# Kernel optimization log

Measured on AMD Instinct MI355X. Metric: run time of the kernel, lower is better.

Reference implementation:

```python
import jax, jax.numpy as jnp
import numpy as np

B, T, D, H = 4, 2048, 1024, 16
HD = D // H  # 64
EPS = 1e-5

def _layernorm(x, g, b):
    mu = jnp.mean(x, axis=-1, keepdims=True)
    var = jnp.var(x, axis=-1, keepdims=True)
    return (x - mu) * jax.lax.rsqrt(var + EPS) * g + b

def setup_inputs() -> dict:
    key = jax.random.key(0)
    ks = jax.random.split(key, 8)
    s = D ** -0.5
    return {
        "x":  jax.random.normal(ks[0], (B, T, D), jnp.float32),
        "Wq": jax.random.normal(ks[1], (H, D, HD), jnp.float32) * s,
        "Wk": jax.random.normal(ks[2], (H, D, HD), jnp.float32) * s,
        "Wv": jax.random.normal(ks[3], (H, D, HD), jnp.float32) * s,
        "Wp": jax.random.normal(ks[4], (D, D), jnp.float32) * s,
        "bp": jnp.zeros((D,), jnp.float32),
        "W1": jax.random.normal(ks[5], (D, 4 * D), jnp.float32) * s,
        "b1": jnp.zeros((4 * D,), jnp.float32),
        "W2": jax.random.normal(ks[6], (4 * D, D), jnp.float32) * (4 * D) ** -0.5,
        "b2": jnp.zeros((D,), jnp.float32),
        "g1": jnp.ones((D,), jnp.float32),
        "be1": jnp.zeros((D,), jnp.float32),
        "g2": jnp.ones((D,), jnp.float32),
        "be2": jnp.zeros((D,), jnp.float32),
    }

def reference(x, Wq, Wk, Wv, Wp, bp, W1, b1, W2, b2, g1, be1, g2, be2):
    # --- pre-LN causal MHA (all heads batched; torch code loops per head) ---
    h = _layernorm(x, g1, be1)                       # [B,T,D]
    q = jnp.einsum('btd,hdk->bhtk', h, Wq)
    k = jnp.einsum('btd,hdk->bhtk', h, Wk)
    v = jnp.einsum('btd,hdk->bhtk', h, Wv)
    scores = jnp.einsum('bhtk,bhsk->bhts', q, k) * (HD ** -0.5)
    causal = jnp.tril(jnp.ones((T, T), bool))
    scores = jnp.where(causal, scores, -jnp.inf)
    w = jax.nn.softmax(scores, axis=-1)              # [B,H,T,T]
    o = jnp.einsum('bhts,bhsk->bhtk', w, v)          # [B,H,T,HD]
    o = o.transpose(0, 2, 1, 3).reshape(x.shape[0], x.shape[1], D)  # concat heads
    x = x + o @ Wp + bp                              # residual 1
    # --- pre-LN FFN ---
    h2 = _layernorm(x, g2, be2)
    ff = jax.nn.relu(h2 @ W1 + b1) @ W2 + b2
    return x + ff
```

## Files before the change

kernel.cpp:

```cpp
#include <hip/hip_runtime.h>
#include <hip/hip_bf16.h>
#include <math.h>

#define Bsz 4
#define Tsz 2048
#define Dsz 1024
#define Hn  16
#define HDs 64

typedef __attribute__((ext_vector_type(8))) short bf16x8;
typedef __attribute__((ext_vector_type(4))) float f32x4;

typedef const __attribute__((address_space(1))) void gvoid;
typedef __attribute__((address_space(3))) void lvoid;

__device__ __forceinline__ void async_copy16(const short* g, short* l) {
    __builtin_amdgcn_global_load_lds((gvoid*)g, (lvoid*)l, 16, 0, 0);
}

__device__ __forceinline__ short f2bf(float x) {
    __hip_bfloat16 h = __float2bfloat16(x);
    return *reinterpret_cast<short*>(&h);
}

__device__ __forceinline__ unsigned int pack_bf16(float hi, float lo) {
    unsigned int uh = __float_as_uint(hi) + 0x8000u;
    unsigned int ul = __float_as_uint(lo) + 0x8000u;
    return __builtin_amdgcn_perm(uh, ul, 0x07060302u);
}

__device__ __forceinline__ size_t headed_idx(int m, int c) {
    int b = m >> 11, t = m & 2047, h = c >> 6, kc = c & 63;
    return (((size_t)(b * Hn + h) * Tsz + t) << 6) + kc;
}

__global__ __launch_bounds__(256) void ln_kernel(const float* __restrict__ x,
                                                 const float* __restrict__ g,
                                                 const float* __restrict__ beta,
                                                 short* __restrict__ out)
{
    const int row = blockIdx.x;
    const float* xr = x + (size_t)row * Dsz;
    float v[4];
    float s = 0.f, s2 = 0.f;
#pragma unroll
    for (int i = 0; i < 4; ++i) {
        v[i] = xr[threadIdx.x + 256 * i];
        s += v[i];
        s2 += v[i] * v[i];
    }
#pragma unroll
    for (int off = 32; off; off >>= 1) {
        s  += __shfl_xor(s,  off);
        s2 += __shfl_xor(s2, off);
    }
    __shared__ float red[8];
    const int wave = threadIdx.x >> 6;
    if ((threadIdx.x & 63) == 0) { red[wave * 2] = s; red[wave * 2 + 1] = s2; }
    __syncthreads();
    s  = red[0] + red[2] + red[4] + red[6];
    s2 = red[1] + red[3] + red[5] + red[7];
    const float mu  = s * (1.f / Dsz);
    const float var = s2 * (1.f / Dsz) - mu * mu;
    const float rs  = rsqrtf(var + 1e-5f);
    short* orow = out + (size_t)row * Dsz;
#pragma unroll
    for (int i = 0; i < 4; ++i) {
        int col = threadIdx.x + 256 * i;
        orow[col] = f2bf((v[i] - mu) * rs * g[col] + beta[col]);
    }
}

__global__ __launch_bounds__(256) void transpose_cvt(
    const float* __restrict__ in, short* __restrict__ outp, int R, int C)
{
    __shared__ float tile[32][33];
    const int r0 = blockIdx.y * 32, c0 = blockIdx.x * 32;
    const size_t so = (size_t)blockIdx.z * R * C;
    const int tx = threadIdx.x & 31, ty = threadIdx.x >> 5;
    const float* ip = in + so;
    short* op = outp + so;
#pragma unroll
    for (int i = 0; i < 4; ++i)
        tile[ty + i * 8][tx] = ip[(size_t)(r0 + ty + i * 8) * C + c0 + tx];
    __syncthreads();
#pragma unroll
    for (int i = 0; i < 4; ++i)
        op[(size_t)(c0 + ty + i * 8) * R + r0 + tx] = f2bf(tile[tx][ty + i * 8]);
}

__global__ __launch_bounds__(256) void transpose_cvt_qkv(
    const float* __restrict__ Wq, const float* __restrict__ Wk,
    const float* __restrict__ Wv, short* __restrict__ outp)
{
    __shared__ float tile[32][33];
    const int z = blockIdx.z;
    const float* in = (z < 16) ? Wq : (z < 32) ? Wk : Wv;
    const int zz = z & 15;
    const int r0 = blockIdx.y * 32, c0 = blockIdx.x * 32;
    const int tx = threadIdx.x & 31, ty = threadIdx.x >> 5;
    const float* ip = in + (size_t)zz * (1024 * 64);
    short* op = outp + (size_t)z * (1024 * 64);
#pragma unroll
    for (int i = 0; i < 4; ++i)
        tile[ty + i * 8][tx] = ip[(size_t)(r0 + ty + i * 8) * 64 + c0 + tx];
    __syncthreads();
#pragma unroll
    for (int i = 0; i < 4; ++i)
        op[(size_t)(c0 + ty + i * 8) * 1024 + r0 + tx] = f2bf(tile[tx][ty + i * 8]);
}

template <int EPI>
__global__ __launch_bounds__(256) void gemm_mfma(
    const short* __restrict__ A, const short* __restrict__ Bt,
    const float* __restrict__ bias, const float* __restrict__ resid,
    float* __restrict__ Cf, short* __restrict__ Cb0,
    short* __restrict__ Cb1, short* __restrict__ Cb2,
    int M, int N, int K, float scale)
{
    __shared__ short As[2][128 * 32];
    __shared__ short Bs[2][128 * 32];
    const int tid  = threadIdx.x;
    const int lane = tid & 63, wave = tid >> 6;
    const int quad = lane >> 4, l16 = lane & 15;

    const int lin = blockIdx.y * gridDim.x + blockIdx.x;
    const int xcd = lin & 7;
    const int s   = lin >> 3;
    const int my  = xcd * 8 + (s & 7);
    const int nx  = s >> 3;
    const int m0 = my * 128, n0 = nx * 128;

    const int wm = (wave >> 1) * 64, wn = (wave & 1) * 64;

    f32x4 acc[4][4];
#pragma unroll
    for (int i = 0; i < 4; ++i)
#pragma unroll
        for (int j = 0; j < 4; ++j) acc[i][j] = f32x4{0.f, 0.f, 0.f, 0.f};

    const short* gA = A  + (size_t)(m0 + wave * 32 + (lane >> 2)) * K + (lane & 3) * 8;
    const short* gB = Bt + (size_t)(n0 + wave * 32 + (lane >> 2)) * K + (lane & 3) * 8;
    const size_t rstep = (size_t)16 * K;
    const int woff = wave * 1024;

    async_copy16(gA,         &As[0][woff]);
    async_copy16(gA + rstep, &As[0][woff + 512]);
    async_copy16(gB,         &Bs[0][woff]);
    async_copy16(gB + rstep, &Bs[0][woff + 512]);
    gA += 32; gB += 32;
    __syncthreads();

    int cur = 0;
    for (int k0 = 0; k0 < K; k0 += 32) {
        if (k0 + 32 < K) {
            const int nxt = cur ^ 1;
            async_copy16(gA,         &As[nxt][woff]);
            async_copy16(gA + rstep, &As[nxt][woff + 512]);
            async_copy16(gB,         &Bs[nxt][woff]);
            async_copy16(gB + rstep, &Bs[nxt][woff + 512]);
            gA += 32; gB += 32;
        }
        bf16x8 af[4], bfr[4];
#pragma unroll
        for (int mt = 0; mt < 4; ++mt)
            af[mt] = *(const bf16x8*)(&As[cur][(wm + mt * 16 + l16) * 32 + quad * 8]);
#pragma unroll
        for (int nt = 0; nt < 4; ++nt)
            bfr[nt] = *(const bf16x8*)(&Bs[cur][(wn + nt * 16 + l16) * 32 + quad * 8]);
#pragma unroll
        for (int mt = 0; mt < 4; ++mt)
#pragma unroll
            for (int nt = 0; nt < 4; ++nt)
                acc[mt][nt] = __builtin_amdgcn_mfma_f32_16x16x32_bf16(
                    af[mt], bfr[nt], acc[mt][nt], 0, 0, 0);
        __syncthreads();
        cur ^= 1;
    }

#pragma unroll
    for (int mt = 0; mt < 4; ++mt) {
#pragma unroll
        for (int nt = 0; nt < 4; ++nt) {
#pragma unroll
            for (int r = 0; r < 4; ++r) {
                const int m = m0 + wm + mt * 16 + quad * 4 + r;
                const int c = n0 + wn + nt * 16 + l16;
                float val = acc[mt][nt][r];
                if (EPI == 0) {
                    const int sel = c >> 10, cl = c & 1023;
                    if (sel == 0)
                        Cb0[headed_idx(m, cl)] = f2bf(val * scale);
                    else if (sel == 1)
                        Cb1[headed_idx(m, cl)] = f2bf(val);
                    else {
                        int b = m >> 11, t = m & 2047;
                        size_t idx = ((((size_t)((b << 4) | (cl >> 6)) << 6) | (cl & 63)) << 11) | t;
                        Cb2[idx] = f2bf(val);
                    }
                } else if (EPI == 2) {
                    size_t idx = (size_t)m * N + c;
                    Cf[idx] = val + bias[c] + resid[idx];
                } else {
                    float v2 = val + bias[c];
                    Cb0[(size_t)m * N + c] = f2bf(v2 > 0.f ? v2 : 0.f);
                }
            }
        }
    }
}

__global__ __launch_bounds__(256) void gemm_n64(
    const short* __restrict__ A, const short* __restrict__ Bt,
    const float* __restrict__ bias, const float* __restrict__ resid,
    float* __restrict__ Cf, int M, int N, int K)
{
    __shared__ short As[2][128 * 64];
    __shared__ short Bs[2][64 * 64];
    const int tid  = threadIdx.x;
    const int lane = tid & 63, wave = tid >> 6;
    const int quad = lane >> 4, l16 = lane & 15;

    const int lin = blockIdx.y * 16 + blockIdx.x;
    const int xcd = lin & 7;
    const int s   = lin >> 3;
    const int m0  = (xcd * 8 + (s & 7)) * 128;
    const int n0  = (s >> 3) * 64;

    const int wm = (wave >> 1) * 64, wn = (wave & 1) * 32;

    f32x4 acc[4][2];
#pragma unroll
    for (int i = 0; i < 4; ++i)
#pragma unroll
        for (int j = 0; j < 2; ++j) acc[i][j] = f32x4{0.f, 0.f, 0.f, 0.f};

    const short* gA[4];
    const short* gB[2];
    int dA[4], dB[2];
#pragma unroll
    for (int i = 0; i < 4; ++i) {
        const int sl = tid + 256 * i, r = sl >> 3, g = (sl & 7) ^ (r & 7);
        gA[i] = A + (size_t)(m0 + r) * K + g * 8;
        dA[i] = sl * 8;
    }
#pragma unroll
    for (int i = 0; i < 2; ++i) {
        const int sl = tid + 256 * i, r = sl >> 3, g = (sl & 7) ^ (r & 7);
        gB[i] = Bt + (size_t)(n0 + r) * K + g * 8;
        dB[i] = sl * 8;
    }

#pragma unroll
    for (int i = 0; i < 4; ++i) { async_copy16(gA[i], &As[0][dA[i]]); gA[i] += 64; }
#pragma unroll
    for (int i = 0; i < 2; ++i) { async_copy16(gB[i], &Bs[0][dB[i]]); gB[i] += 64; }
    __syncthreads();

    int cur = 0;
    for (int k0 = 0; k0 < K; k0 += 64) {
        if (k0 + 64 < K) {
            const int nxt = cur ^ 1;
#pragma unroll
            for (int i = 0; i < 4; ++i) { async_copy16(gA[i], &As[nxt][dA[i]]); gA[i] += 64; }
#pragma unroll
            for (int i = 0; i < 2; ++i) { async_copy16(gB[i], &Bs[nxt][dB[i]]); gB[i] += 64; }
        }
        bf16x8 af[4][2], bfr[2][2];
#pragma unroll
        for (int mt = 0; mt < 4; ++mt) {
            const int r = wm + mt * 16 + l16;
            af[mt][0] = *(const bf16x8*)(&As[cur][r * 64 + (((quad    ) ^ (r & 7)) << 3)]);
            af[mt][1] = *(const bf16x8*)(&As[cur][r * 64 + (((quad + 4) ^ (r & 7)) << 3)]);
        }
#pragma unroll
        for (int nt = 0; nt < 2; ++nt) {
            const int r = wn + nt * 16 + l16;
            bfr[nt][0] = *(const bf16x8*)(&Bs[cur][r * 64 + (((quad    ) ^ (r & 7)) << 3)]);
            bfr[nt][1] = *(const bf16x8*)(&Bs[cur][r * 64 + (((quad + 4) ^ (r & 7)) << 3)]);
        }
#pragma unroll
        for (int mt = 0; mt < 4; ++mt)
#pragma unroll
            for (int nt = 0; nt < 2; ++nt) {
                acc[mt][nt] = __builtin_amdgcn_mfma_f32_16x16x32_bf16(
                    af[mt][0], bfr[nt][0], acc[mt][nt], 0, 0, 0);
                acc[mt][nt] = __builtin_amdgcn_mfma_f32_16x16x32_bf16(
                    af[mt][1], bfr[nt][1], acc[mt][nt], 0, 0, 0);
            }
        __syncthreads();
        cur ^= 1;
    }

#pragma unroll
    for (int mt = 0; mt < 4; ++mt) {
#pragma unroll
        for (int nt = 0; nt < 2; ++nt) {
#pragma unroll
            for (int r = 0; r < 4; ++r) {
                const int m = m0 + wm + mt * 16 + quad * 4 + r;
                const int c = n0 + wn + nt * 16 + l16;
                const size_t idx = (size_t)m * N + c;
                Cf[idx] = acc[mt][nt][r] + bias[c] + resid[idx];
            }
        }
    }
}

__global__ __launch_bounds__(256, 4) void fattn_kernel(
    const short* __restrict__ Q,
    const short* __restrict__ K,
    const short* __restrict__ VT,
    short* __restrict__ O)
{
    __shared__ short Kl[2][64 * 64];
    __shared__ short Vl[2][64 * 64];
    __shared__ short p_lds[4][16 * 64];
    const int tid  = threadIdx.x;
    const int lane = tid & 63, wave = tid >> 6;
    const int quad = lane >> 4, l16 = lane & 15;

    const int lin  = blockIdx.y * 16 + blockIdx.x;
    const int xcd  = lin & 7;
    const int slot = lin >> 3;
    const int bh   = xcd * 8 + (slot >> 4);
    const int px   = slot & 15;
    const int tiles[2] = { 31 - px, px };

    const int bb = bh >> 4, hh = bh & 15;
    const size_t bhoff = (size_t)bh * (Tsz * HDs);
    const short* Qb = Q + bhoff;
    const short* Kb = K + bhoff;
    const short* Vb = VT + bhoff;

    const int s_a = tid, s_b = tid + 256;
    const int ra = s_a >> 3, ga = (s_a & 7) ^ (ra & 7);
    const int rb = s_b >> 3, gb = (s_b & 7) ^ (rb & 7);

    short* pw = &p_lds[wave][0];
    const int rd0 = l16 * 64 + (((quad    ) ^ (l16 & 7)) << 3);
    const int rd1 = l16 * 64 + (((quad + 4) ^ (l16 & 7)) << 3);

    bf16x8 bq[2][2];
#pragma unroll
    for (int ti = 0; ti < 2; ++ti) {
        const short* qp = Qb + (size_t)(tiles[ti] * 64 + wave * 16 + l16) * 64 + quad * 8;
        bq[ti][0] = *(const bf16x8*)qp;
        bq[ti][1] = *(const bf16x8*)(qp + 32);
    }

    auto stage = [&](int c64, int buf) {
        short* kb_l = &Kl[buf][0];
        short* vb_l = &Vl[buf][0];
        async_copy16(Kb + (((size_t)(c64 + ra)) << 6) + (ga << 3), kb_l + s_a * 8);
        async_copy16(Kb + (((size_t)(c64 + rb)) << 6) + (gb << 3), kb_l + s_b * 8);
        async_copy16(Vb + ((size_t)ra << 11) + c64 + (ga << 3), vb_l + s_a * 8);
        async_copy16(Vb + ((size_t)rb << 11) + c64 + (gb << 3), vb_l + s_b * 8);
    };

    stage(tiles[0] * 0, 0);
    __syncthreads();

    int phase = 0;
#pragma unroll
    for (int ti = 0; ti < 2; ++ti) {
        const int tile = tiles[ti];
        const int q0w  = tile * 64 + wave * 16;
        const int nch  = tile + 1;

        f32x4 oaccT[4];
        float lacc = 0.f;
#pragma unroll
        for (int nt = 0; nt < 4; ++nt) oaccT[nt] = f32x4{0.f, 0.f, 0.f, 0.f};

        for (int c = 0; c < nch; ++c) {
            const int cur = phase & 1;
            if (c + 1 < nch)   stage((c + 1) * 64, cur ^ 1);
            else if (ti == 0)  stage(0, cur ^ 1);

            const int s0 = c * 64;
            const short* Kc = &Kl[cur][0];
            const short* Vc = &Vl[cur][0];
            bf16x8 ak[4][2], av[4][2];
#pragma unroll
            for (int ct = 0; ct < 4; ++ct) {
                const int r = ct * 16 + l16;
                ak[ct][0] = *(const bf16x8*)(Kc + r * 64 + (((quad    ) ^ (r & 7)) << 3));
                ak[ct][1] = *(const bf16x8*)(Kc + r * 64 + (((quad + 4) ^ (r & 7)) << 3));
            }
#pragma unroll
            for (int nt = 0; nt < 4; ++nt) {
                const int r = nt * 16 + l16;
                av[nt][0] = *(const bf16x8*)(Vc + r * 64 + (((quad    ) ^ (r & 7)) << 3));
                av[nt][1] = *(const bf16x8*)(Vc + r * 64 + (((quad + 4) ^ (r & 7)) << 3));
            }
            f32x4 sfr[4];
#pragma unroll
            for (int ct = 0; ct < 4; ++ct) {
                f32x4 cc = {0.f, 0.f, 0.f, 0.f};
                cc = __builtin_amdgcn_mfma_f32_16x16x32_bf16(ak[ct][0], bq[ti][0], cc, 0, 0, 0);
                cc = __builtin_amdgcn_mfma_f32_16x16x32_bf16(ak[ct][1], bq[ti][1], cc, 0, 0, 0);
                sfr[ct] = cc;
            }
            if (s0 + 63 > q0w) {
                const int qr = q0w + l16;
#pragma unroll
                for (int ct = 0; ct < 4; ++ct)
#pragma unroll
                    for (int r = 0; r < 4; ++r)
                        if (s0 + ct * 16 + quad * 4 + r > qr)
                            sfr[ct][r] = -INFINITY;
            }
#pragma unroll
            for (int ct = 0; ct < 4; ++ct) {
                float p0 = __builtin_exp2f(sfr[ct][0]);
                float p1 = __builtin_exp2f(sfr[ct][1]);
                float p2 = __builtin_exp2f(sfr[ct][2]);
                float p3 = __builtin_exp2f(sfr[ct][3]);
                lacc += (p0 + p1) + (p2 + p3);
                uint2 pkv;
                pkv.x = pack_bf16(p1, p0);
                pkv.y = pack_bf16(p3, p2);
                const int g = (2 * ct + (quad >> 1)) ^ (l16 & 7);
                *(uint2*)(pw + l16 * 64 + (g << 3) + (quad & 1) * 4) = pkv;
            }
            bf16x8 bp0 = *(const bf16x8*)(pw + rd0);
            bf16x8 bp1 = *(const bf16x8*)(pw + rd1);
#pragma unroll
            for (int nt = 0; nt < 4; ++nt) {
                oaccT[nt] = __builtin_amdgcn_mfma_f32_16x16x32_bf16(av[nt][0], bp0, oaccT[nt], 0, 0, 0);
                oaccT[nt] = __builtin_amdgcn_mfma_f32_16x16x32_bf16(av[nt][1], bp1, oaccT[nt], 0, 0, 0);
            }
            __syncthreads();
            ++phase;
        }

        float ps = lacc;
        ps += __shfl_xor(ps, 16);
        ps += __shfl_xor(ps, 32);
        const float inv = 1.f / ps;
        short* orow = O + (size_t)(bb * Tsz + q0w + l16) * Dsz + hh * 64;
#pragma unroll
        for (int nt = 0; nt < 4; ++nt) {
            uint2 pkv;
            pkv.x = pack_bf16(oaccT[nt][1] * inv, oaccT[nt][0] * inv);
            pkv.y = pack_bf16(oaccT[nt][3] * inv, oaccT[nt][2] * inv);
            *(uint2*)(orow + nt * 16 + quad * 4) = pkv;
        }
    }
}

extern "C" void kernel_launch(void* const* d_in, const int* in_sizes, int n_in,
                              void* d_out, int out_size, void* d_ws, size_t ws_size,
                              hipStream_t stream) {
    const float* x   = (const float*)d_in[0];
    const float* Wq  = (const float*)d_in[1];
    const float* Wk  = (const float*)d_in[2];
    const float* Wv  = (const float*)d_in[3];
    const float* Wp  = (const float*)d_in[4];
    const float* bp  = (const float*)d_in[5];
    const float* W1  = (const float*)d_in[6];
    const float* b1  = (const float*)d_in[7];
    const float* W2  = (const float*)d_in[8];
    const float* b2  = (const float*)d_in[9];
    const float* g1  = (const float*)d_in[10];
    const float* be1 = (const float*)d_in[11];
    const float* g2  = (const float*)d_in[12];
    const float* be2 = (const float*)d_in[13];
    float* out = (float*)d_out;
    char*  W   = (char*)d_ws;

    short* h1  = (short*)(W);
    short* ff1 = (short*)(W);
    short* qb  = (short*)(W + (16ull << 20));
    short* kb  = (short*)(W + (32ull << 20));
    short* vtb = (short*)(W + (48ull << 20));
    short* o   = (short*)(W + (64ull << 20));
    short* h2  = (short*)(W + (80ull << 20));
    short* wqt = (short*)(W + (96ull << 20));
    short* wpt = (short*)(W + (102ull << 20));
    short* w1t = (short*)(W + (104ull << 20));
    short* w2t = (short*)(W + (112ull << 20));

    const int M = Bsz * Tsz;
    const float qscale = 0.125f * 1.44269504f;

    transpose_cvt_qkv<<<dim3(2, 32, 48), 256, 0, stream>>>(Wq, Wk, Wv, wqt);
    transpose_cvt<<<dim3(32, 32, 1),  256, 0, stream>>>(Wp, wpt, 1024, 1024);
    transpose_cvt<<<dim3(128, 32, 1), 256, 0, stream>>>(W1, w1t, 1024, 4096);
    transpose_cvt<<<dim3(32, 128, 1), 256, 0, stream>>>(W2, w2t, 4096, 1024);

    ln_kernel<<<dim3(M), 256, 0, stream>>>(x, g1, be1, h1);

    gemm_mfma<0><<<dim3(24, 64), 256, 0, stream>>>(
        h1, wqt, nullptr, nullptr, nullptr, qb, kb, vtb, M, 3072, 1024, qscale);

    fattn_kernel<<<dim3(16, Bsz * Hn), 256, 0, stream>>>(qb, kb, vtb, o);

    gemm_n64<<<dim3(16, 64), 256, 0, stream>>>(
        o, wpt, bp, x, out, M, 1024, 1024);

    ln_kernel<<<dim3(M), 256, 0, stream>>>(out, g2, be2, h2);

    gemm_mfma<3><<<dim3(32, 64), 256, 0, stream>>>(
        h2, w1t, b1, nullptr, nullptr, ff1, nullptr, nullptr, M, 4096, 1024, 1.f);

    gemm_n64<<<dim3(16, 64), 256, 0, stream>>>(
        ff1, w2t, b2, out, out, M, 1024, 4096);
}
```

Before: 537.9 us.

## Prefetch two K-tiles ahead with explicit vmcnt waits in both GEMM kernels

```diff
diff --git a/kernel.cpp b/kernel.cpp
--- a/kernel.cpp
+++ b/kernel.cpp
@@ -144,49 +144,59 @@
     const size_t rstep = (size_t)16 * K;
     const int woff = wave * 1024;
 
-    async_copy16(gA,         &As[0][woff]);
-    async_copy16(gA + rstep, &As[0][woff + 512]);
-    async_copy16(gB,         &Bs[0][woff]);
-    async_copy16(gB + rstep, &Bs[0][woff + 512]);
-    gA += 32; gB += 32;
-    __syncthreads();
-
+    auto stageg = [&](int buf) {
+        async_copy16(gA,         &As[buf][woff]);
+        async_copy16(gA + rstep, &As[buf][woff + 512]);
+        async_copy16(gB,         &Bs[buf][woff]);
+        async_copy16(gB + rstep, &Bs[buf][woff + 512]);
+        gA += 32; gB += 32;
+    };
+
+    stageg(0);
+    stageg(1);
+
+    const int ntile = K >> 5;
     int cur = 0;
-    for (int k0 = 0; k0 < K; k0 += 32) {
-        if (k0 + 32 < K) {
-            const int nxt = cur ^ 1;
-            async_copy16(gA,         &As[nxt][woff]);
-            async_copy16(gA + rstep, &As[nxt][woff + 512]);
-            async_copy16(gB,         &Bs[nxt][woff]);
-            async_copy16(gB + rstep, &Bs[nxt][woff + 512]);
-            gA += 32; gB += 32;
-        }
+    for (int t = 0; t < ntile; ++t) {
+        if (t + 1 < ntile) asm volatile("s_waitcnt vmcnt(4)" ::: "memory");
+        else               asm volatile("s_waitcnt vmcnt(0)" ::: "memory");
+        __builtin_amdgcn_s_barrier();
+        __builtin_amdgcn_sched_barrier(0);
+
         bf16x8 af[4], bfr[4];
 #pragma unroll
         for (int mt = 0; mt < 4; ++mt)
             af[mt] = *(const bf16x8*)(&As[cur][(wm + mt * 16 + l16) * 32 + quad * 8]);
 #pragma unroll
-        for (int nt = 0; nt < 4; ++nt)
-            bfr[nt] = *(const bf16x8*)(&Bs[cur][(wn + nt * 16 + l16) * 32 + quad * 8]);
+        for (int nt2 = 0; nt2 < 4; ++nt2)
+            bfr[nt2] = *(const bf16x8*)(&Bs[cur][(wn + nt2 * 16 + l16) * 32 + quad * 8]);
+
+        if (t + 2 < ntile) {
+            asm volatile("s_waitcnt lgkmcnt(0)" ::: "memory");
+            __builtin_amdgcn_sched_barrier(0);
+            __builtin_amdgcn_s_barrier();
+            __builtin_amdgcn_sched_barrier(0);
+            stageg(cur);
+        }
+
 #pragma unroll
         for (int mt = 0; mt < 4; ++mt)
 #pragma unroll
-            for (int nt = 0; nt < 4; ++nt)
-                acc[mt][nt] = __builtin_amdgcn_mfma_f32_16x16x32_bf16(
-                    af[mt], bfr[nt], acc[mt][nt], 0, 0, 0);
-        __syncthreads();
+            for (int nt2 = 0; nt2 < 4; ++nt2)
+                acc[mt][nt2] = __builtin_amdgcn_mfma_f32_16x16x32_bf16(
+                    af[mt], bfr[nt2], acc[mt][nt2], 0, 0, 0);
         cur ^= 1;
     }
 
 #pragma unroll
     for (int mt = 0; mt < 4; ++mt) {
 #pragma unroll
-        for (int nt = 0; nt < 4; ++nt) {
+        for (int nt2 = 0; nt2 < 4; ++nt2) {
 #pragma unroll
             for (int r = 0; r < 4; ++r) {
                 const int m = m0 + wm + mt * 16 + quad * 4 + r;
-                const int c = n0 + wn + nt * 16 + l16;
-                float val = acc[mt][nt][r];
+                const int c = n0 + wn + nt2 * 16 + l16;
+                float val = acc[mt][nt2][r];
                 if (EPI == 0) {
                     const int sel = c >> 10, cl = c & 1023;
                     if (sel == 0)
@@ -251,21 +261,24 @@
         dB[i] = sl * 8;
     }
 
-#pragma unroll
-    for (int i = 0; i < 4; ++i) { async_copy16(gA[i], &As[0][dA[i]]); gA[i] += 64; }
-#pragma unroll
-    for (int i = 0; i < 2; ++i) { async_copy16(gB[i], &Bs[0][dB[i]]); gB[i] += 64; }
-    __syncthreads();
-
+    auto stageg = [&](int buf) {
+#pragma unroll
+        for (int i = 0; i < 4; ++i) { async_copy16(gA[i], &As[buf][dA[i]]); gA[i] += 64; }
+#pragma unroll
+        for (int i = 0; i < 2; ++i) { async_copy16(gB[i], &Bs[buf][dB[i]]); gB[i] += 64; }
+    };
+
+    stageg(0);
+    stageg(1);
+
+    const int ntile = K >> 6;
     int cur = 0;
-    for (int k0 = 0; k0 < K; k0 += 64) {
-        if (k0 + 64 < K) {
-            const int nxt = cur ^ 1;
-#pragma unroll
-            for (int i = 0; i < 4; ++i) { async_copy16(gA[i], &As[nxt][dA[i]]); gA[i] += 64; }
-#pragma unroll
-            for (int i = 0; i < 2; ++i) { async_copy16(gB[i], &Bs[nxt][dB[i]]); gB[i] += 64; }
-        }
+    for (int t = 0; t < ntile; ++t) {
+        if (t + 1 < ntile) asm volatile("s_waitcnt vmcnt(6)" ::: "memory");
+        else               asm volatile("s_waitcnt vmcnt(0)" ::: "memory");
+        __builtin_amdgcn_s_barrier();
+        __builtin_amdgcn_sched_barrier(0);
+
         bf16x8 af[4][2], bfr[2][2];
 #pragma unroll
         for (int mt = 0; mt < 4; ++mt) {
@@ -274,34 +287,42 @@
             af[mt][1] = *(const bf16x8*)(&As[cur][r * 64 + (((quad + 4) ^ (r & 7)) << 3)]);
         }
 #pragma unroll
-        for (int nt = 0; nt < 2; ++nt) {
-            const int r = wn + nt * 16 + l16;
-            bfr[nt][0] = *(const bf16x8*)(&Bs[cur][r * 64 + (((quad    ) ^ (r & 7)) << 3)]);
-            bfr[nt][1] = *(const bf16x8*)(&Bs[cur][r * 64 + (((quad + 4) ^ (r & 7)) << 3)]);
-        }
+        for (int nt2 = 0; nt2 < 2; ++nt2) {
+            const int r = wn + nt2 * 16 + l16;
+            bfr[nt2][0] = *(const bf16x8*)(&Bs[cur][r * 64 + (((quad    ) ^ (r & 7)) << 3)]);
+            bfr[nt2][1] = *(const bf16x8*)(&Bs[cur][r * 64 + (((quad + 4) ^ (r & 7)) << 3)]);
+        }
+
+        if (t + 2 < ntile) {
+            asm volatile("s_waitcnt lgkmcnt(0)" ::: "memory");
+            __builtin_amdgcn_sched_barrier(0);
+            __builtin_amdgcn_s_barrier();
+            __builtin_amdgcn_sched_barrier(0);
+            stageg(cur);
+        }
+
 #pragma unroll
         for (int mt = 0; mt < 4; ++mt)
 #pragma unroll
-            for (int nt = 0; nt < 2; ++nt) {
-                acc[mt][nt] = __builtin_amdgcn_mfma_f32_16x16x32_bf16(
-                    af[mt][0], bfr[nt][0], acc[mt][nt], 0, 0, 0);
-                acc[mt][nt] = __builtin_amdgcn_mfma_f32_16x16x32_bf16(
-                    af[mt][1], bfr[nt][1], acc[mt][nt], 0, 0, 0);
-            }
-        __syncthreads();
+            for (int nt2 = 0; nt2 < 2; ++nt2) {
+                acc[mt][nt2] = __builtin_amdgcn_mfma_f32_16x16x32_bf16(
+                    af[mt][0], bfr[nt2][0], acc[mt][nt2], 0, 0, 0);
+                acc[mt][nt2] = __builtin_amdgcn_mfma_f32_16x16x32_bf16(
+                    af[mt][1], bfr[nt2][1], acc[mt][nt2], 0, 0, 0);
+            }
         cur ^= 1;
     }
 
 #pragma unroll
     for (int mt = 0; mt < 4; ++mt) {
 #pragma unroll
-        for (int nt = 0; nt < 2; ++nt) {
+        for (int nt2 = 0; nt2 < 2; ++nt2) {
 #pragma unroll
             for (int r = 0; r < 4; ++r) {
                 const int m = m0 + wm + mt * 16 + quad * 4 + r;
-                const int c = n0 + wn + nt * 16 + l16;
+                const int c = n0 + wn + nt2 * 16 + l16;
                 const size_t idx = (size_t)m * N + c;
-                Cf[idx] = acc[mt][nt][r] + bias[c] + resid[idx];
+                Cf[idx] = acc[mt][nt2][r] + bias[c] + resid[idx];
             }
         }
     }
```

Result: faster. 513.6 us (-4.5%).
